# Performance work log

Hardware: AMD Instinct MI355X
Metric: run time of the kernel (lower is better)

Reference implementation:

```python
import jax, jax.numpy as jnp
from jax import lax
import numpy as np

VOCAB, TAGS, EMBED, HIDDEN, BATCH, SEQ = 50000, 9, 300, 1000, 32, 200


def setup_inputs() -> dict:
    key = jax.random.key(0)
    ks = jax.random.split(key, 12)
    s_e = 1.0 / np.sqrt(HIDDEN)
    inp = {
        "x": jax.random.randint(ks[0], (SEQ, BATCH), 0, VOCAB),
        "y": jax.random.randint(ks[1], (SEQ, BATCH), 0, TAGS),
        "embed_w": jax.random.normal(ks[2], (VOCAB, EMBED), jnp.float32),
        "W_ih": jax.random.uniform(ks[3], (4 * HIDDEN, EMBED), jnp.float32, -s_e, s_e),
        "W_hh": jax.random.uniform(ks[4], (4 * HIDDEN, HIDDEN), jnp.float32, -s_e, s_e),
        "b_ih": jax.random.uniform(ks[5], (4 * HIDDEN,), jnp.float32, -s_e, s_e),
        "b_hh": jax.random.uniform(ks[6], (4 * HIDDEN,), jnp.float32, -s_e, s_e),
        "lin_w": jax.random.uniform(ks[7], (TAGS, HIDDEN), jnp.float32, -s_e, s_e),
        "lin_b": jax.random.uniform(ks[8], (TAGS,), jnp.float32, -s_e, s_e),
        "start_trans": jax.random.uniform(ks[9], (TAGS,), jnp.float32, -0.1, 0.1),
        "end_trans": jax.random.uniform(ks[10], (TAGS,), jnp.float32, -0.1, 0.1),
        "trans": jax.random.uniform(ks[11], (TAGS, TAGS), jnp.float32, -0.1, 0.1),
    }
    return inp


def _forward(x, y, embed_w, W_ih, W_hh, b_ih, b_hh, lin_w, lin_b, start_trans, end_trans, trans):
    T, B = x.shape
    H = W_hh.shape[1]
    embeds = embed_w[x]  # [T,B,E]
    # Precompute input contribution to gates: [T,B,4H]
    xg = jnp.einsum("tbe,ge->tbg", embeds, W_ih) + b_ih + b_hh

    def lstm_step(carry, xg_t):
        h, c = carry
        g = xg_t + h @ W_hh.T  # [B,4H]
        i, f, gg, o = jnp.split(g, 4, axis=-1)  # PyTorch gate order i,f,g,o
        c = jax.nn.sigmoid(f) * c + jax.nn.sigmoid(i) * jnp.tanh(gg)
        h = jax.nn.sigmoid(o) * jnp.tanh(c)
        return (h, c), h

    h0 = jnp.zeros((B, H), embeds.dtype)
    _, hs = lax.scan(lstm_step, (h0, h0), xg)  # hs: [T,B,H]

    tag_space = jnp.einsum("tbh,kh->tbk", hs, lin_w) + lin_b  # [T,B,K]
    # Faithful to original: log_softmax over dim=1 (the batch axis)
    emissions = jax.nn.log_softmax(tag_space, axis=1)

    # ---- CRF log-likelihood (pytorch-crf semantics, full mask, sum reduction) ----
    b_idx = jnp.arange(B)
    em_at_y = jnp.take_along_axis(emissions, y[:, :, None], axis=2)[:, :, 0]  # [T,B]
    numerator = (
        start_trans[y[0]]
        + em_at_y.sum(axis=0)
        + trans[y[:-1], y[1:]].sum(axis=0)
        + end_trans[y[-1]]
    )  # [B]

    alpha0 = start_trans[None, :] + emissions[0]  # [B,K]

    def crf_step(alpha, em_t):
        # alpha: [B,K] over previous tag; em_t: [B,K]
        nxt = jax.nn.logsumexp(alpha[:, :, None] + trans[None, :, :] + em_t[:, None, :], axis=1)
        return nxt, None

    alpha, _ = lax.scan(crf_step, alpha0, emissions[1:])
    log_z = jax.nn.logsumexp(alpha + end_trans[None, :], axis=1)  # [B]
    return (numerator - log_z).sum()


def reference(x, y, embed_w, W_ih, W_hh, b_ih, b_hh, lin_w, lin_b, start_trans, end_trans, trans):
    return _forward(x, y, embed_w, W_ih, W_hh, b_ih, b_hh, lin_w, lin_b, start_trans, end_trans, trans)
```

## Files before the change

kernel.cpp:

```cpp
#include <hip/hip_runtime.h>

#define T_SEQ 200
#define NB    32
#define NE    300
#define NH    1000
#define NK    9
#define NJ    4096
#define EPD   320
#define WSCALE 256.0f
#define HSCALE 16.0f
#define LSCALE 512.0f
#define GSCALE (1.0f / (256.0f * 16.0f))
#define TSCALE (1.0f / (16.0f * 512.0f))

typedef __attribute__((ext_vector_type(4))) float f32x4;
typedef __attribute__((ext_vector_type(8))) short s16x8;
typedef __attribute__((ext_vector_type(4))) short s16x4;
typedef unsigned long long u64;

__device__ __forceinline__ unsigned short f2bf(float f) {
    union { float f; unsigned u; } v; v.f = f;
    unsigned r = v.u + 0x7FFFu + ((v.u >> 16) & 1u);
    return (unsigned short)(r >> 16);
}
__device__ __forceinline__ float bf2f(unsigned short h) {
    union { unsigned u; float f; } v; v.u = ((unsigned)h) << 16;
    return v.f;
}
__device__ __forceinline__ float ftanh(float x) {
    float e = __expf(fminf(2.f * x, 80.f));
    return (e - 1.f) / (e + 1.f);
}
__device__ __forceinline__ float fsig(float x) {
    return 1.f / (1.f + __expf(-x));
}
__device__ __forceinline__ unsigned nt_poll(const unsigned* p) {
    unsigned r;
    asm volatile("global_load_dword %0, %1, off nt\n\t"
                 "s_waitcnt vmcnt(0)"
                 : "=v"(r) : "v"(p) : "memory");
    return r;
}
__device__ __forceinline__ void plain_pub(unsigned* p, unsigned v) {
    __hip_atomic_store(p, v, __ATOMIC_RELAXED, __HIP_MEMORY_SCOPE_WORKGROUP);
}

__global__ __launch_bounds__(256) void prep_emb(
    const int* __restrict__ x, const float* __restrict__ embed_w,
    unsigned short* __restrict__ emb_bf, unsigned* __restrict__ ctrl)
{
    const int t = blockIdx.x, tid = threadIdx.x;
    if (blockIdx.x == 0) {
        for (int i = tid; i < 2048; i += 256)
            ctrl[i] = (i == 61) ? 0xffffffffu : 0u;
    }
    for (int idx = tid; idx < NB * EPD; idx += 256) {
        int b = idx / EPD, e = idx - b * EPD;
        float v = (e < NE) ? embed_w[(size_t)x[t * NB + b] * NE + e] : 0.f;
        emb_bf[((size_t)t * NB + b) * EPD + e] = f2bf(v);
    }
}

__global__ __launch_bounds__(256) void prep_w(
    const float* __restrict__ W_ih, const float* __restrict__ b_ih,
    const float* __restrict__ b_hh, const float* __restrict__ lin_w,
    unsigned short* __restrict__ wih_bf, float* __restrict__ biasg,
    unsigned char* __restrict__ linw_q)
{
    const int blk = blockIdx.x, tid = threadIdx.x;
    for (int idx = tid; idx < 64 * EPD; idx += 256) {
        int jr = idx / EPD, e = idx - jr * EPD;
        int jp = blk * 64 + jr;
        int wgu = jp >> 7, rr = jp & 127, g = rr >> 5, uu = rr & 31;
        int m = wgu * 32 + uu;
        float v = (m < NH && e < NE) ? W_ih[(size_t)(g * NH + m) * NE + e] : 0.f;
        wih_bf[(size_t)jp * EPD + e] = f2bf(v);
    }
    if (tid < 64) {
        int jp = blk * 64 + tid;
        int wgu = jp >> 7, rr = jp & 127, g = rr >> 5, uu = rr & 31;
        int m = wgu * 32 + uu;
        biasg[jp] = (m < NH) ? (b_ih[g * NH + m] + b_hh[g * NH + m]) : 0.f;
    }
    if (blk < 16) {
        int n = blk, k = tid * 4;
        float v0 = (n < NK && k + 0 < NH) ? lin_w[(size_t)n * NH + k + 0] * LSCALE : 0.f;
        float v1 = (n < NK && k + 1 < NH) ? lin_w[(size_t)n * NH + k + 1] * LSCALE : 0.f;
        float v2 = (n < NK && k + 2 < NH) ? lin_w[(size_t)n * NH + k + 2] * LSCALE : 0.f;
        float v3 = (n < NK && k + 3 < NH) ? lin_w[(size_t)n * NH + k + 3] * LSCALE : 0.f;
        int p01 = __builtin_amdgcn_cvt_pk_fp8_f32(v0, v1, 0, false);
        int p23 = __builtin_amdgcn_cvt_pk_fp8_f32(v2, v3, 0, false);
        ((unsigned*)linw_q)[n * 256 + tid] =
            ((unsigned)p01 & 0xffffu) | ((unsigned)p23 << 16);
    }
}

__device__ __forceinline__ int gate_xg(unsigned* done, int ready, int tn, int lane) {
    while (ready <= tn) {
        unsigned v = 64u;
        if (lane < 8 && ready + lane < T_SEQ)
            v = __hip_atomic_load(&done[ready + lane], __ATOMIC_RELAXED,
                                  __HIP_MEMORY_SCOPE_AGENT);
        unsigned m = (unsigned)__ballot((int)(v >= 64u)) & 255u;
        if (m & 1u) {
            unsigned run = (m == 255u) ? 8u : (unsigned)__builtin_ctz(~m);
            ready += (int)run;
        } else {
            __builtin_amdgcn_s_sleep(1);
        }
    }
    return ready;
}

__global__ __launch_bounds__(256, 1) void lstm_kernel(
    const float* __restrict__ W_hh,
    const unsigned short* __restrict__ emb_bf,
    const unsigned short* __restrict__ wih_bf,
    const float* __restrict__ biasg,
    unsigned short* __restrict__ xg,
    unsigned char* __restrict__ h_q,
    unsigned* __restrict__ ctrl)
{
    __shared__ __align__(16) unsigned char s_w[128 * 1024];
    __shared__ int s_chunk, s_grp, s_pid, s_mode;

    const int tid = threadIdx.x;

    if (tid == 0) {
        unsigned xcc;
        asm volatile("s_getreg_b32 %0, hwreg(HW_REG_XCC_ID)" : "=s"(xcc));
        xcc &= 15u;
        unsigned myidx = __hip_atomic_fetch_add(&ctrl[40 + xcc], 1u,
                             __ATOMIC_RELAXED, __HIP_MEMORY_SCOPE_AGENT);
        __threadfence();
        unsigned tot = __hip_atomic_fetch_add(&ctrl[60], 1u,
                             __ATOMIC_RELAXED, __HIP_MEMORY_SCOPE_AGENT);
        if (tot == 255u) {
            __threadfence();
            unsigned w0 = 0xffu, w1 = 0xffu;
            for (unsigned xx = 0; xx < 16; ++xx) {
                unsigned cx = __hip_atomic_load(&ctrl[40 + xx], __ATOMIC_RELAXED,
                                                __HIP_MEMORY_SCOPE_AGENT);
                if (cx >= 32u) {
                    if (w0 == 0xffu) w0 = xx;
                    else { w1 = xx; break; }
                }
            }
            __hip_atomic_store(&ctrl[61], w0 | (w1 << 8), __ATOMIC_RELAXED,
                               __HIP_MEMORY_SCOPE_AGENT);
        }
        unsigned win;
        do {
            win = __hip_atomic_load(&ctrl[61], __ATOMIC_RELAXED,
                                    __HIP_MEMORY_SCOPE_AGENT);
        } while (win == 0xffffffffu);
        unsigned w0 = win & 0xffu, w1 = (win >> 8) & 0xffu;
        int grp = -1;
        if (xcc == w0 && myidx < 32u) grp = 0;
        else if (xcc == w1 && myidx < 32u) grp = 1;
        s_grp = grp;
        s_chunk = (grp >= 0) ? (int)myidx : -1;
        s_pid = (grp >= 0) ? -1
                     : (int)__hip_atomic_fetch_add(&ctrl[62], 1u,
                           __ATOMIC_RELAXED, __HIP_MEMORY_SCOPE_AGENT);
    }
    __syncthreads();
    const int chunk = s_chunk;
    const int w = tid >> 6, lane = tid & 63;
    const int col = lane & 15, quad = lane >> 4;
    unsigned* done = ctrl + 256;

    if (chunk < 0) {
        const int pid = s_pid;
        for (int g = pid; g < T_SEQ * 64; g += 192) {
            const int t = g >> 6, jt = g & 63;
            const unsigned short* eb = emb_bf + (size_t)t * NB * EPD;
            const unsigned short* wb = wih_bf + (size_t)(jt * 64 + w * 16 + col) * EPD;
            const unsigned short* ea0 = eb + (size_t)col * EPD;
            const unsigned short* ea1 = eb + (size_t)(16 + col) * EPD;

            f32x4 acc0 = {0.f, 0.f, 0.f, 0.f};
            f32x4 acc1 = {0.f, 0.f, 0.f, 0.f};
#pragma unroll
            for (int kc = 0; kc < EPD / 32; ++kc) {
                int ko = kc * 32 + quad * 8;
                s16x8 a0 = *(const s16x8*)&ea0[ko];
                s16x8 a1 = *(const s16x8*)&ea1[ko];
                s16x8 bb = *(const s16x8*)&wb[ko];
                acc0 = __builtin_amdgcn_mfma_f32_16x16x32_bf16(a0, bb, acc0, 0, 0, 0);
                acc1 = __builtin_amdgcn_mfma_f32_16x16x32_bf16(a1, bb, acc1, 0, 0, 0);
            }
            const int jp = jt * 64 + w * 16 + col;
            const float bi = biasg[jp];
            size_t base = ((size_t)t * NJ + jp) * NB;
            union { s16x4 v; u64 q; } p0, p1;
#pragma unroll
            for (int r = 0; r < 4; ++r) {
                p0.v[r] = (short)f2bf(acc0[r] + bi);
                p1.v[r] = (short)f2bf(acc1[r] + bi);
            }
            __hip_atomic_store((u64*)&xg[base + quad * 4], p0.q,
                               __ATOMIC_RELAXED, __HIP_MEMORY_SCOPE_AGENT);
            __hip_atomic_store((u64*)&xg[base + 16 + quad * 4], p1.q,
                               __ATOMIC_RELAXED, __HIP_MEMORY_SCOPE_AGENT);
            __syncthreads();
            if (tid == 0)
                __hip_atomic_fetch_add(&done[t], 1u, __ATOMIC_RELAXED,
                                       __HIP_MEMORY_SCOPE_AGENT);
        }
        return;
    }

    const int grp = s_grp;
    const size_t GOFF = (size_t)grp * 16384;
    unsigned* fastf = ctrl + 64 + grp * 64;
    unsigned* slowf = ctrl + grp * 96;
    unsigned* s_w32 = (unsigned*)s_w;

    for (int idx = tid; idx < 128 * 256; idx += 256) {
        int r = idx >> 8, dw = idx & 255;
        int g = r >> 5, uu = r & 31, m = chunk * 32 + uu;
        float4 w4 = make_float4(0.f, 0.f, 0.f, 0.f);
        if (m < NH && dw < 250)
            w4 = *(const float4*)&W_hh[(size_t)(g * NH + m) * NH + dw * 4];
        int p0 = __builtin_amdgcn_cvt_pk_fp8_f32(w4.x * WSCALE, w4.y * WSCALE, 0, false);
        int p1 = __builtin_amdgcn_cvt_pk_fp8_f32(w4.z * WSCALE, w4.w * WSCALE, 0, false);
        unsigned v = ((unsigned)p0 & 0xffffu) | ((unsigned)p1 << 16);
        int kb = dw >> 1;
        int kbs = kb ^ (r & 15);
        s_w32[r * 256 + (kbs << 1) + (dw & 1)] = v;
    }
    if (tid < 128)
        *(unsigned*)(h_q + GOFF + (size_t)chunk * 512 + tid * 4) = 0u;
    __syncthreads();
    if (tid == 0) {
        plain_pub(&fastf[chunk], 1u);
        __hip_atomic_store(&slowf[chunk], 1u, __ATOMIC_RELAXED,
                           __HIP_MEMORY_SCOPE_AGENT);
    }
    if (grp == 0 && chunk == 0) {
        if (tid < 64) {
            int mode = 2;
            for (int it = 0; it < 8192; ++it) {
                unsigned v = (lane < 32) ? nt_poll(&fastf[lane]) : 1u;
                if (__all((int)(v >= 1u))) { mode = 1; break; }
            }
            if (tid == 0) {
                __hip_atomic_store(&ctrl[63], (unsigned)mode, __ATOMIC_RELAXED,
                                   __HIP_MEMORY_SCOPE_AGENT);
                s_mode = mode;
            }
        }
    } else {
        if (tid == 0) {
            unsigned m;
            do {
                m = __hip_atomic_load(&ctrl[63], __ATOMIC_RELAXED,
                                      __HIP_MEMORY_SCOPE_AGENT);
            } while (m == 0u);
            s_mode = (int)m;
        }
    }
    __syncthreads();
    const int mode = s_mode;

    if (w >= 2) {
        for (int t = 0; t < T_SEQ; ++t) __syncthreads();
        return;
    }
    const int p = w;

    int ready = 0;
    ready = gate_xg(done, ready, 0, lane);
    s16x4 xcur[4], xnxt[4];
#pragma unroll
    for (int g = 0; g < 4; ++g)
        xcur[g] = *(const s16x4*)&xg[((size_t)0 * NJ + chunk * 128 + (2 * g + p) * 16 + col) * NB
                                     + grp * 16 + quad * 4];

    float c[4] = {0.f, 0.f, 0.f, 0.f};
    const int rw = quad * 4;
    const int boff = col * 32 + quad * 8;

    for (int t = 0; t < T_SEQ; ++t) {
        const unsigned need = (unsigned)(t + 1);
        if (mode == 1) {
            for (;;) {
                unsigned v = (lane < 32) ? nt_poll(&fastf[lane]) : need;
                if (__all((int)(v >= need))) break;
            }
        } else {
            for (;;) {
                unsigned v = (lane < 32)
                    ? __hip_atomic_load(&slowf[lane], __ATOMIC_RELAXED,
                                        __HIP_MEMORY_SCOPE_AGENT)
                    : need;
                if (__all((int)(v >= need))) break;
            }
        }
        asm volatile("" ::: "memory");

        const unsigned char* pb = h_q + (size_t)t * 32768 + GOFF + boff;
        u64 a[32];
#pragma unroll
        for (int kc = 0; kc < 32; ++kc)
            a[kc] = *(const u64*)(pb + (size_t)kc * 512);

        if (t + 1 < T_SEQ) {
            ready = gate_xg(done, ready, t + 1, lane);
#pragma unroll
            for (int g = 0; g < 4; ++g)
                xnxt[g] = *(const s16x4*)&xg[((size_t)(t + 1) * NJ + chunk * 128 + (2 * g + p) * 16 + col) * NB
                                             + grp * 16 + quad * 4];
        }

        f32x4 acc0 = {0.f, 0.f, 0.f, 0.f};
        f32x4 acc1 = {0.f, 0.f, 0.f, 0.f};
        f32x4 acc2 = {0.f, 0.f, 0.f, 0.f};
        f32x4 acc3 = {0.f, 0.f, 0.f, 0.f};
#pragma unroll
        for (int kc = 0; kc < 32; ++kc) {
            int kb = kc * 4 + quad;
            u64 b0 = *(const u64*)&s_w[((0 * 2 + p) * 16 + col) * 1024 + ((kb ^ col) << 3)];
            u64 b1 = *(const u64*)&s_w[((1 * 2 + p) * 16 + col) * 1024 + ((kb ^ col) << 3)];
            u64 b2 = *(const u64*)&s_w[((2 * 2 + p) * 16 + col) * 1024 + ((kb ^ col) << 3)];
            u64 b3 = *(const u64*)&s_w[((3 * 2 + p) * 16 + col) * 1024 + ((kb ^ col) << 3)];
            acc0 = __builtin_amdgcn_mfma_f32_16x16x32_fp8_fp8((long)a[kc], (long)b0, acc0, 0, 0, 0);
            acc1 = __builtin_amdgcn_mfma_f32_16x16x32_fp8_fp8((long)a[kc], (long)b1, acc1, 0, 0, 0);
            acc2 = __builtin_amdgcn_mfma_f32_16x16x32_fp8_fp8((long)a[kc], (long)b2, acc2, 0, 0, 0);
            acc3 = __builtin_amdgcn_mfma_f32_16x16x32_fp8_fp8((long)a[kc], (long)b3, acc3, 0, 0, 0);
        }

        float hv[4];
#pragma unroll
        for (int r = 0; r < 4; ++r) {
            float gi = acc0[r] * GSCALE + bf2f((unsigned short)xcur[0][r]);
            float gf = acc1[r] * GSCALE + bf2f((unsigned short)xcur[1][r]);
            float gg = acc2[r] * GSCALE + bf2f((unsigned short)xcur[2][r]);
            float go = acc3[r] * GSCALE + bf2f((unsigned short)xcur[3][r]);
            c[r] = fsig(gf) * c[r] + fsig(gi) * ftanh(gg);
            hv[r] = fsig(go) * ftanh(c[r]);
        }
        {
            int p01 = __builtin_amdgcn_cvt_pk_fp8_f32(hv[0] * HSCALE, hv[1] * HSCALE, 0, false);
            int p23 = __builtin_amdgcn_cvt_pk_fp8_f32(hv[2] * HSCALE, hv[3] * HSCALE, 0, false);
            unsigned char* pg = h_q + (size_t)(t + 1) * 32768 + GOFF + (size_t)chunk * 512
                              + p * 16 + col;
            pg[(rw + 0) * 32] = (unsigned char)(p01 & 0xff);
            pg[(rw + 1) * 32] = (unsigned char)((p01 >> 8) & 0xff);
            pg[(rw + 2) * 32] = (unsigned char)(p23 & 0xff);
            pg[(rw + 3) * 32] = (unsigned char)((p23 >> 8) & 0xff);
        }
        __syncthreads();
        if (tid == 0) {
            plain_pub(&fastf[chunk], (unsigned)(t + 2));
            if (mode == 2)
                __hip_atomic_store(&slowf[chunk], (unsigned)(t + 2),
                                   __ATOMIC_RELAXED, __HIP_MEMORY_SCOPE_AGENT);
        }
#pragma unroll
        for (int g = 0; g < 4; ++g) xcur[g] = xnxt[g];
    }
}

__global__ __launch_bounds__(64) void tag_gemm(
    const unsigned char* __restrict__ h_q,
    const unsigned char* __restrict__ linw_q, float* __restrict__ ts)
{
    const int m0 = blockIdx.x * 16, lane = threadIdx.x;
    const int col = lane & 15, quad = lane >> 4;
    const int m = m0 + col, t = m >> 5, b = m & 31;
    const int g = b >> 4, bl = b & 15;
    const unsigned char* pa = h_q + (size_t)(t + 1) * 32768 + (size_t)g * 16384
                            + bl * 32 + quad * 8;
    const unsigned char* pw = linw_q + (size_t)col * 1024 + quad * 8;

    f32x4 acc = {0.f, 0.f, 0.f, 0.f};
#pragma unroll 8
    for (int kc = 0; kc < 32; ++kc) {
        u64 a  = *(const u64*)(pa + (size_t)kc * 512);
        u64 bv = *(const u64*)(pw + kc * 32);
        acc = __builtin_amdgcn_mfma_f32_16x16x32_fp8_fp8((long)a, (long)bv, acc, 0, 0, 0);
    }
#pragma unroll
    for (int r = 0; r < 4; ++r)
        ts[(size_t)(m0 + quad * 4 + r) * 16 + col] = acc[r] * TSCALE;
}

__global__ __launch_bounds__(320) void em_kernel(
    const float* __restrict__ ts, const float* __restrict__ lin_b,
    float* __restrict__ em)
{
    __shared__ float s_ts[NB * NK];
    __shared__ float s_lse[NK];
    const int t = blockIdx.x, tid = threadIdx.x;
    float val = 0.f;
    int b = tid / NK, k = tid - b * NK;
    if (tid < NB * NK) {
        val = ts[(size_t)(t * NB + b) * 16 + k] + lin_b[k];
        s_ts[b * NK + k] = val;
    }
    __syncthreads();
    if (tid < NK) {
        float m = -1e30f;
        for (int bb = 0; bb < NB; ++bb) m = fmaxf(m, s_ts[bb * NK + tid]);
        float s = 0.f;
        for (int bb = 0; bb < NB; ++bb) s += __expf(s_ts[bb * NK + tid] - m);
        s_lse[tid] = m + __logf(s);
    }
    __syncthreads();
    if (tid < NB * NK)
        em[((size_t)t * NB + b) * NK + k] = val - s_lse[k];
}

__global__ __launch_bounds__(320) void crf_kernel(
    const int* __restrict__ y, const float* __restrict__ em,
    const float* __restrict__ start_trans, const float* __restrict__ end_trans,
    const float* __restrict__ trans, float* __restrict__ out)
{
    __shared__ float s_trans[NK * NK];
    __shared__ float s_alpha[NB * NK];
    __shared__ float s_red[NB];
    const int tid = threadIdx.x;
    if (tid < NK * NK) s_trans[tid] = trans[tid];
    __syncthreads();

    float num = 0.f;
    if (tid < NB) {
        int b = tid, yp = y[b];
        num = start_trans[yp] + em[(size_t)b * NK + yp];
        for (int t = 1; t < T_SEQ; ++t) {
            int yc = y[t * NB + b];
            num += s_trans[yp * NK + yc] + em[((size_t)t * NB + b) * NK + yc];
            yp = yc;
        }
        num += end_trans[yp];
    }

    const int b = tid / NK, k = tid - (tid / NK) * NK;
    if (tid < NB * NK)
        s_alpha[tid] = start_trans[k] + em[(size_t)b * NK + k];
    __syncthreads();

    for (int t = 1; t < T_SEQ; ++t) {
        float nv = 0.f;
        if (tid < NB * NK) {
            float m = -1e30f;
#pragma unroll
            for (int i = 0; i < NK; ++i)
                m = fmaxf(m, s_alpha[b * NK + i] + s_trans[i * NK + k]);
            float s = 0.f;
#pragma unroll
            for (int i = 0; i < NK; ++i)
                s += __expf(s_alpha[b * NK + i] + s_trans[i * NK + k] - m);
            nv = em[((size_t)t * NB + b) * NK + k] + m + __logf(s);
        }
        __syncthreads();
        if (tid < NB * NK) s_alpha[tid] = nv;
        __syncthreads();
    }

    if (tid < NB) {
        float m = -1e30f;
        for (int k2 = 0; k2 < NK; ++k2)
            m = fmaxf(m, s_alpha[tid * NK + k2] + end_trans[k2]);
        float s = 0.f;
        for (int k2 = 0; k2 < NK; ++k2)
            s += __expf(s_alpha[tid * NK + k2] + end_trans[k2] - m);
        s_red[tid] = num - (m + __logf(s));
    }
    __syncthreads();
    if (tid == 0) {
        float tot = 0.f;
        for (int i = 0; i < NB; ++i) tot += s_red[i];
        out[0] = tot;
    }
}

extern "C" void kernel_launch(void* const* d_in, const int* in_sizes, int n_in,
                              void* d_out, int out_size, void* d_ws, size_t ws_size,
                              hipStream_t stream)
{
    const int*   x           = (const int*)d_in[0];
    const int*   y           = (const int*)d_in[1];
    const float* embed_w     = (const float*)d_in[2];
    const float* W_ih        = (const float*)d_in[3];
    const float* W_hh        = (const float*)d_in[4];
    const float* b_ih        = (const float*)d_in[5];
    const float* b_hh        = (const float*)d_in[6];
    const float* lin_w       = (const float*)d_in[7];
    const float* lin_b       = (const float*)d_in[8];
    const float* start_trans = (const float*)d_in[9];
    const float* end_trans   = (const float*)d_in[10];
    const float* trans       = (const float*)d_in[11];
    float* out = (float*)d_out;

    char* ws = (char*)d_ws;
    unsigned short* xg     = (unsigned short*)(ws);
    float*          ts     = (float*)(ws);
    unsigned char*  h_q    = (unsigned char*)(ws + 52428800);
    unsigned char*  linw_q = (unsigned char*)(ws + 59015168);
    float*          em     = (float*)(ws + 65601536);
    unsigned*       ctrl   = (unsigned*)(ws + 65831936);
    float*          biasg  = (float*)(ws + 65840128);
    unsigned short* emb_bf = (unsigned short*)(ws + 65856512);
    unsigned short* wih_bf = (unsigned short*)(ws + 69952512);

    prep_emb<<<dim3(T_SEQ), 256, 0, stream>>>(x, embed_w, emb_bf, ctrl);
    prep_w<<<dim3(64), 256, 0, stream>>>(W_ih, b_ih, b_hh, lin_w, wih_bf, biasg, linw_q);

    lstm_kernel<<<dim3(256), 256, 0, stream>>>(W_hh, emb_bf, wih_bf, biasg,
                                               xg, h_q, ctrl);

    tag_gemm<<<dim3(400), 64, 0, stream>>>(h_q, linw_q, ts);
    em_kernel<<<dim3(T_SEQ), 320, 0, stream>>>(ts, lin_b, em);
    crf_kernel<<<dim3(1), 320, 0, stream>>>(y, em, start_trans, end_trans, trans, out);
}
```

Before: 1.040 ms.

## Replace per-chunk flag polling with L2 atomic counter and offload xg prefetch to idle waves

Cross-block step synchronization now uses a single per-group counter incremented with an L2 atomic add and polled by one wave with sleeps, instead of 32 lanes polling per-chunk flags. The previously idle waves 2-3 prefetch the next step's input-gate values into a double-buffered LDS tile, so the compute waves no longer do global xg loads. This adds an extra __syncthreads per step and always writes the slow flag as a fallback. The intent is less poll traffic and a shorter critical path per recurrent step.

```diff
diff --git a/kernel.cpp b/kernel.cpp
--- a/kernel.cpp
+++ b/kernel.cpp
@@ -34,15 +34,16 @@
 __device__ __forceinline__ float fsig(float x) {
     return 1.f / (1.f + __expf(-x));
 }
-__device__ __forceinline__ unsigned nt_poll(const unsigned* p) {
+__device__ __forceinline__ void l2_add1(unsigned* p) {
+    asm volatile("global_atomic_add %0, %1, off"
+                 :: "v"(p), "v"(1u) : "memory");
+}
+__device__ __forceinline__ unsigned l2_poll(const unsigned* p) {
     unsigned r;
-    asm volatile("global_load_dword %0, %1, off nt\n\t"
+    asm volatile("global_load_dword %0, %1, off sc0 nt\n\t"
                  "s_waitcnt vmcnt(0)"
                  : "=v"(r) : "v"(p) : "memory");
     return r;
-}
-__device__ __forceinline__ void plain_pub(unsigned* p, unsigned v) {
-    __hip_atomic_store(p, v, __ATOMIC_RELAXED, __HIP_MEMORY_SCOPE_WORKGROUP);
 }
 
 __global__ __launch_bounds__(256) void prep_emb(
@@ -122,6 +123,7 @@
     unsigned* __restrict__ ctrl)
 {
     __shared__ __align__(16) unsigned char s_w[128 * 1024];
+    __shared__ __align__(16) unsigned char s_xg[2][4096];
     __shared__ int s_chunk, s_grp, s_pid, s_mode;
 
     const int tid = threadIdx.x;
@@ -213,8 +215,8 @@
 
     const int grp = s_grp;
     const size_t GOFF = (size_t)grp * 16384;
-    unsigned* fastf = ctrl + 64 + grp * 64;
     unsigned* slowf = ctrl + grp * 96;
+    unsigned* cnt   = ctrl + 64 + grp * 96;
     unsigned* s_w32 = (unsigned*)s_w;
 
     for (int idx = tid; idx < 128 * 256; idx += 256) {
@@ -234,21 +236,21 @@
         *(unsigned*)(h_q + GOFF + (size_t)chunk * 512 + tid * 4) = 0u;
     __syncthreads();
     if (tid == 0) {
-        plain_pub(&fastf[chunk], 1u);
+        l2_add1(cnt);
         __hip_atomic_store(&slowf[chunk], 1u, __ATOMIC_RELAXED,
                            __HIP_MEMORY_SCOPE_AGENT);
     }
     if (grp == 0 && chunk == 0) {
-        if (tid < 64) {
-            int mode = 2;
-            for (int it = 0; it < 8192; ++it) {
-                unsigned v = (lane < 32) ? nt_poll(&fastf[lane]) : 1u;
-                if (__all((int)(v >= 1u))) { mode = 1; break; }
+        if (w == 0) {
+            int md = 2;
+            for (int it = 0; it < 4096; ++it) {
+                if (l2_poll(cnt) >= 32u) { md = 1; break; }
+                __builtin_amdgcn_s_sleep(1);
             }
             if (tid == 0) {
-                __hip_atomic_store(&ctrl[63], (unsigned)mode, __ATOMIC_RELAXED,
+                __hip_atomic_store(&ctrl[63], (unsigned)md, __ATOMIC_RELAXED,
                                    __HIP_MEMORY_SCOPE_AGENT);
-                s_mode = mode;
+                s_mode = md;
             }
         }
     } else {
@@ -264,102 +266,120 @@
     __syncthreads();
     const int mode = s_mode;
 
-    if (w >= 2) {
-        for (int t = 0; t < T_SEQ; ++t) __syncthreads();
-        return;
-    }
-    const int p = w;
-
-    int ready = 0;
-    ready = gate_xg(done, ready, 0, lane);
-    s16x4 xcur[4], xnxt[4];
-#pragma unroll
-    for (int g = 0; g < 4; ++g)
-        xcur[g] = *(const s16x4*)&xg[((size_t)0 * NJ + chunk * 128 + (2 * g + p) * 16 + col) * NB
-                                     + grp * 16 + quad * 4];
-
+    const int p = w & 1;
     float c[4] = {0.f, 0.f, 0.f, 0.f};
     const int rw = quad * 4;
     const int boff = col * 32 + quad * 8;
+    int ready23 = 0;
+
+    if (w >= 2) {
+        ready23 = gate_xg(done, 0, 0, lane);
+        const int idx128 = tid - 128;
+        const size_t rb = ((size_t)0 * NJ + chunk * 128 + idx128) * NB + grp * 16;
+        unsigned char* db = &s_xg[0][idx128 * 32];
+#pragma unroll
+        for (int bq = 0; bq < 4; ++bq)
+            *(u64*)(db + bq * 8) = *(const u64*)&xg[rb + bq * 4];
+    }
 
     for (int t = 0; t < T_SEQ; ++t) {
-        const unsigned need = (unsigned)(t + 1);
-        if (mode == 1) {
-            for (;;) {
-                unsigned v = (lane < 32) ? nt_poll(&fastf[lane]) : need;
-                if (__all((int)(v >= need))) break;
+        if (w == 0) {
+            const unsigned need = (unsigned)(t + 1);
+            if (mode == 1) {
+                const unsigned need32 = 32u * need;
+                int it = 0;
+                for (;;) {
+                    if (l2_poll(cnt) >= need32) break;
+                    if (++it >= 65536) {
+                        unsigned v = (lane < 32)
+                            ? __hip_atomic_load(&slowf[lane], __ATOMIC_RELAXED,
+                                                __HIP_MEMORY_SCOPE_AGENT)
+                            : need;
+                        if (__all((int)(v >= need))) break;
+                        it = 0;
+                    }
+                    __builtin_amdgcn_s_sleep(1);
+                }
+            } else {
+                for (;;) {
+                    unsigned v = (lane < 32)
+                        ? __hip_atomic_load(&slowf[lane], __ATOMIC_RELAXED,
+                                            __HIP_MEMORY_SCOPE_AGENT)
+                        : need;
+                    if (__all((int)(v >= need))) break;
+                }
+            }
+            asm volatile("" ::: "memory");
+        }
+        __syncthreads();
+
+        if (w < 2) {
+            const unsigned char* pb = h_q + (size_t)t * 32768 + GOFF + boff;
+            u64 a[32];
+#pragma unroll
+            for (int kc = 0; kc < 32; ++kc)
+                a[kc] = *(const u64*)(pb + (size_t)kc * 512);
+
+            f32x4 acc0 = {0.f, 0.f, 0.f, 0.f};
+            f32x4 acc1 = {0.f, 0.f, 0.f, 0.f};
+            f32x4 acc2 = {0.f, 0.f, 0.f, 0.f};
+            f32x4 acc3 = {0.f, 0.f, 0.f, 0.f};
+#pragma unroll
+            for (int kc = 0; kc < 32; ++kc) {
+                int kb = kc * 4 + quad;
+                u64 b0 = *(const u64*)&s_w[((0 * 2 + p) * 16 + col) * 1024 + ((kb ^ col) << 3)];
+                u64 b1 = *(const u64*)&s_w[((1 * 2 + p) * 16 + col) * 1024 + ((kb ^ col) << 3)];
+                u64 b2 = *(const u64*)&s_w[((2 * 2 + p) * 16 + col) * 1024 + ((kb ^ col) << 3)];
+                u64 b3 = *(const u64*)&s_w[((3 * 2 + p) * 16 + col) * 1024 + ((kb ^ col) << 3)];
+                acc0 = __builtin_amdgcn_mfma_f32_16x16x32_fp8_fp8((long)a[kc], (long)b0, acc0, 0, 0, 0);
+                acc1 = __builtin_amdgcn_mfma_f32_16x16x32_fp8_fp8((long)a[kc], (long)b1, acc1, 0, 0, 0);
+                acc2 = __builtin_amdgcn_mfma_f32_16x16x32_fp8_fp8((long)a[kc], (long)b2, acc2, 0, 0, 0);
+                acc3 = __builtin_amdgcn_mfma_f32_16x16x32_fp8_fp8((long)a[kc], (long)b3, acc3, 0, 0, 0);
+            }
+
+            const unsigned char* xb = &s_xg[t & 1][0];
+            s16x4 xc[4];
+#pragma unroll
+            for (int g = 0; g < 4; ++g)
+                xc[g] = *(const s16x4*)&xb[(((2 * g + p) * 16 + col) * 32) + quad * 8];
+
+            float hv[4];
+#pragma unroll
+            for (int r = 0; r < 4; ++r) {
+                float gi = acc0[r] * GSCALE + bf2f((unsigned short)xc[0][r]);
+                float gf = acc1[r] * GSCALE + bf2f((unsigned short)xc[1][r]);
+                float gg = acc2[r] * GSCALE + bf2f((unsigned short)xc[2][r]);
+                float go = acc3[r] * GSCALE + bf2f((unsigned short)xc[3][r]);
+                c[r] = fsig(gf) * c[r] + fsig(gi) * ftanh(gg);
+                hv[r] = fsig(go) * ftanh(c[r]);
+            }
+            {
+                int p01 = __builtin_amdgcn_cvt_pk_fp8_f32(hv[0] * HSCALE, hv[1] * HSCALE, 0, false);
+                int p23 = __builtin_amdgcn_cvt_pk_fp8_f32(hv[2] * HSCALE, hv[3] * HSCALE, 0, false);
+                unsigned char* pg = h_q + (size_t)(t + 1) * 32768 + GOFF + (size_t)chunk * 512
+                                  + p * 16 + col;
+                pg[(rw + 0) * 32] = (unsigned char)(p01 & 0xff);
+                pg[(rw + 1) * 32] = (unsigned char)((p01 >> 8) & 0xff);
+                pg[(rw + 2) * 32] = (unsigned char)(p23 & 0xff);
+                pg[(rw + 3) * 32] = (unsigned char)((p23 >> 8) & 0xff);
             }
         } else {
-            for (;;) {
-                unsigned v = (lane < 32)
-                    ? __hip_atomic_load(&slowf[lane], __ATOMIC_RELAXED,
-                                        __HIP_MEMORY_SCOPE_AGENT)
-                    : need;
-                if (__all((int)(v >= need))) break;
-            }
-        }
-        asm volatile("" ::: "memory");
-
-        const unsigned char* pb = h_q + (size_t)t * 32768 + GOFF + boff;
-        u64 a[32];
-#pragma unroll
-        for (int kc = 0; kc < 32; ++kc)
-            a[kc] = *(const u64*)(pb + (size_t)kc * 512);
-
-        if (t + 1 < T_SEQ) {
-            ready = gate_xg(done, ready, t + 1, lane);
-#pragma unroll
-            for (int g = 0; g < 4; ++g)
-                xnxt[g] = *(const s16x4*)&xg[((size_t)(t + 1) * NJ + chunk * 128 + (2 * g + p) * 16 + col) * NB
-                                             + grp * 16 + quad * 4];
-        }
-
-        f32x4 acc0 = {0.f, 0.f, 0.f, 0.f};
-        f32x4 acc1 = {0.f, 0.f, 0.f, 0.f};
-        f32x4 acc2 = {0.f, 0.f, 0.f, 0.f};
-        f32x4 acc3 = {0.f, 0.f, 0.f, 0.f};
-#pragma unroll
-        for (int kc = 0; kc < 32; ++kc) {
-            int kb = kc * 4 + quad;
-            u64 b0 = *(const u64*)&s_w[((0 * 2 + p) * 16 + col) * 1024 + ((kb ^ col) << 3)];
-            u64 b1 = *(const u64*)&s_w[((1 * 2 + p) * 16 + col) * 1024 + ((kb ^ col) << 3)];
-            u64 b2 = *(const u64*)&s_w[((2 * 2 + p) * 16 + col) * 1024 + ((kb ^ col) << 3)];
-            u64 b3 = *(const u64*)&s_w[((3 * 2 + p) * 16 + col) * 1024 + ((kb ^ col) << 3)];
-            acc0 = __builtin_amdgcn_mfma_f32_16x16x32_fp8_fp8((long)a[kc], (long)b0, acc0, 0, 0, 0);
-            acc1 = __builtin_amdgcn_mfma_f32_16x16x32_fp8_fp8((long)a[kc], (long)b1, acc1, 0, 0, 0);
-            acc2 = __builtin_amdgcn_mfma_f32_16x16x32_fp8_fp8((long)a[kc], (long)b2, acc2, 0, 0, 0);
-            acc3 = __builtin_amdgcn_mfma_f32_16x16x32_fp8_fp8((long)a[kc], (long)b3, acc3, 0, 0, 0);
-        }
-
-        float hv[4];
-#pragma unroll
-        for (int r = 0; r < 4; ++r) {
-            float gi = acc0[r] * GSCALE + bf2f((unsigned short)xcur[0][r]);
-            float gf = acc1[r] * GSCALE + bf2f((unsigned short)xcur[1][r]);
-            float gg = acc2[r] * GSCALE + bf2f((unsigned short)xcur[2][r]);
-            float go = acc3[r] * GSCALE + bf2f((unsigned short)xcur[3][r]);
-            c[r] = fsig(gf) * c[r] + fsig(gi) * ftanh(gg);
-            hv[r] = fsig(go) * ftanh(c[r]);
-        }
-        {
-            int p01 = __builtin_amdgcn_cvt_pk_fp8_f32(hv[0] * HSCALE, hv[1] * HSCALE, 0, false);
-            int p23 = __builtin_amdgcn_cvt_pk_fp8_f32(hv[2] * HSCALE, hv[3] * HSCALE, 0, false);
-            unsigned char* pg = h_q + (size_t)(t + 1) * 32768 + GOFF + (size_t)chunk * 512
-                              + p * 16 + col;
-            pg[(rw + 0) * 32] = (unsigned char)(p01 & 0xff);
-            pg[(rw + 1) * 32] = (unsigned char)((p01 >> 8) & 0xff);
-            pg[(rw + 2) * 32] = (unsigned char)(p23 & 0xff);
-            pg[(rw + 3) * 32] = (unsigned char)((p23 >> 8) & 0xff);
+            if (t + 1 < T_SEQ) {
+                ready23 = gate_xg(done, ready23, t + 1, lane);
+                const int idx128 = tid - 128;
+                const size_t rb = ((size_t)(t + 1) * NJ + chunk * 128 + idx128) * NB + grp * 16;
+                unsigned char* db = &s_xg[(t + 1) & 1][idx128 * 32];
+#pragma unroll
+                for (int bq = 0; bq < 4; ++bq)
+                    *(u64*)(db + bq * 8) = *(const u64*)&xg[rb + bq * 4];
+            }
         }
         __syncthreads();
         if (tid == 0) {
-            plain_pub(&fastf[chunk], (unsigned)(t + 2));
-            if (mode == 2)
-                __hip_atomic_store(&slowf[chunk], (unsigned)(t + 2),
-                                   __ATOMIC_RELAXED, __HIP_MEMORY_SCOPE_AGENT);
-        }
-#pragma unroll
-        for (int g = 0; g < 4; ++g) xcur[g] = xnxt[g];
+            l2_add1(cnt);
+            __hip_atomic_store(&slowf[chunk], (unsigned)(t + 2),
+                               __ATOMIC_RELAXED, __HIP_MEMORY_SCOPE_AGENT);
+        }
     }
 }
 
```

Result: slower. 1.194 ms (+14.8%).

## Replace per-step block barrier with per-wave flags and fold xg gating into poll

Applied to the files above, without the earlier changes.

Each of the two active waves in a recurrent block now publishes its own progress flag after a vmcnt wait, instead of the whole block hitting __syncthreads and one thread publishing. The two idle waves simply exit rather than looping through barriers. The xg readiness check is merged into the h-polling spin loop with a two-step lookahead, so it no longer runs as a separate gate. Control words are relocated to avoid overlap with the wider flag arrays. The intent is to shorten the per-timestep critical path of the serial LSTM. The cost is more flags to poll, and correctness now rests on per-wave memory ordering.

```diff
diff --git a/kernel.cpp b/kernel.cpp
--- a/kernel.cpp
+++ b/kernel.cpp
@@ -52,7 +52,7 @@
     const int t = blockIdx.x, tid = threadIdx.x;
     if (blockIdx.x == 0) {
         for (int i = tid; i < 2048; i += 256)
-            ctrl[i] = (i == 61) ? 0xffffffffu : 0u;
+            ctrl[i] = (i == 497) ? 0xffffffffu : 0u;
     }
     for (int idx = tid; idx < NB * EPD; idx += 256) {
         int b = idx / EPD, e = idx - b * EPD;
@@ -130,28 +130,28 @@
         unsigned xcc;
         asm volatile("s_getreg_b32 %0, hwreg(HW_REG_XCC_ID)" : "=s"(xcc));
         xcc &= 15u;
-        unsigned myidx = __hip_atomic_fetch_add(&ctrl[40 + xcc], 1u,
+        unsigned myidx = __hip_atomic_fetch_add(&ctrl[480 + xcc], 1u,
                              __ATOMIC_RELAXED, __HIP_MEMORY_SCOPE_AGENT);
         __threadfence();
-        unsigned tot = __hip_atomic_fetch_add(&ctrl[60], 1u,
+        unsigned tot = __hip_atomic_fetch_add(&ctrl[496], 1u,
                              __ATOMIC_RELAXED, __HIP_MEMORY_SCOPE_AGENT);
         if (tot == 255u) {
             __threadfence();
             unsigned w0 = 0xffu, w1 = 0xffu;
             for (unsigned xx = 0; xx < 16; ++xx) {
-                unsigned cx = __hip_atomic_load(&ctrl[40 + xx], __ATOMIC_RELAXED,
+                unsigned cx = __hip_atomic_load(&ctrl[480 + xx], __ATOMIC_RELAXED,
                                                 __HIP_MEMORY_SCOPE_AGENT);
                 if (cx >= 32u) {
                     if (w0 == 0xffu) w0 = xx;
                     else { w1 = xx; break; }
                 }
             }
-            __hip_atomic_store(&ctrl[61], w0 | (w1 << 8), __ATOMIC_RELAXED,
+            __hip_atomic_store(&ctrl[497], w0 | (w1 << 8), __ATOMIC_RELAXED,
                                __HIP_MEMORY_SCOPE_AGENT);
         }
         unsigned win;
         do {
-            win = __hip_atomic_load(&ctrl[61], __ATOMIC_RELAXED,
+            win = __hip_atomic_load(&ctrl[497], __ATOMIC_RELAXED,
                                     __HIP_MEMORY_SCOPE_AGENT);
         } while (win == 0xffffffffu);
         unsigned w0 = win & 0xffu, w1 = (win >> 8) & 0xffu;
@@ -161,7 +161,7 @@
         s_grp = grp;
         s_chunk = (grp >= 0) ? (int)myidx : -1;
         s_pid = (grp >= 0) ? -1
-                     : (int)__hip_atomic_fetch_add(&ctrl[62], 1u,
+                     : (int)__hip_atomic_fetch_add(&ctrl[498], 1u,
                            __ATOMIC_RELAXED, __HIP_MEMORY_SCOPE_AGENT);
     }
     __syncthreads();
@@ -213,8 +213,8 @@
 
     const int grp = s_grp;
     const size_t GOFF = (size_t)grp * 16384;
-    unsigned* fastf = ctrl + 64 + grp * 64;
-    unsigned* slowf = ctrl + grp * 96;
+    unsigned* slowf = ctrl + grp * 64;
+    unsigned* fastf = ctrl + 128 + grp * 64;
     unsigned* s_w32 = (unsigned*)s_w;
 
     for (int idx = tid; idx < 128 * 256; idx += 256) {
@@ -234,44 +234,40 @@
         *(unsigned*)(h_q + GOFF + (size_t)chunk * 512 + tid * 4) = 0u;
     __syncthreads();
     if (tid == 0) {
-        plain_pub(&fastf[chunk], 1u);
-        __hip_atomic_store(&slowf[chunk], 1u, __ATOMIC_RELAXED,
+        plain_pub(&fastf[chunk * 2 + 0], 1u);
+        plain_pub(&fastf[chunk * 2 + 1], 1u);
+        __hip_atomic_store(&slowf[chunk * 2 + 0], 1u, __ATOMIC_RELAXED,
                            __HIP_MEMORY_SCOPE_AGENT);
-    }
-    if (grp == 0 && chunk == 0) {
-        if (tid < 64) {
-            int mode = 2;
-            for (int it = 0; it < 8192; ++it) {
-                unsigned v = (lane < 32) ? nt_poll(&fastf[lane]) : 1u;
-                if (__all((int)(v >= 1u))) { mode = 1; break; }
-            }
-            if (tid == 0) {
-                __hip_atomic_store(&ctrl[63], (unsigned)mode, __ATOMIC_RELAXED,
-                                   __HIP_MEMORY_SCOPE_AGENT);
-                s_mode = mode;
-            }
-        }
-    } else {
-        if (tid == 0) {
-            unsigned m;
-            do {
-                m = __hip_atomic_load(&ctrl[63], __ATOMIC_RELAXED,
-                                      __HIP_MEMORY_SCOPE_AGENT);
-            } while (m == 0u);
-            s_mode = (int)m;
-        }
+        __hip_atomic_store(&slowf[chunk * 2 + 1], 1u, __ATOMIC_RELAXED,
+                           __HIP_MEMORY_SCOPE_AGENT);
+    }
+    if (grp == 0 && chunk == 0 && w == 0) {
+        int md = 2;
+        for (int it = 0; it < 8192; ++it) {
+            unsigned v = nt_poll(&fastf[lane]);
+            if (__all((int)(v >= 1u))) { md = 1; break; }
+        }
+        if (lane == 0) {
+            __hip_atomic_store(&ctrl[499], (unsigned)md, __ATOMIC_RELAXED,
+                               __HIP_MEMORY_SCOPE_AGENT);
+            s_mode = md;
+        }
+    } else if (tid == 0) {
+        unsigned m;
+        do {
+            m = __hip_atomic_load(&ctrl[499], __ATOMIC_RELAXED,
+                                  __HIP_MEMORY_SCOPE_AGENT);
+        } while (m == 0u);
+        s_mode = (int)m;
     }
     __syncthreads();
     const int mode = s_mode;
 
-    if (w >= 2) {
-        for (int t = 0; t < T_SEQ; ++t) __syncthreads();
-        return;
-    }
+    if (w >= 2) return;
     const int p = w;
-
-    int ready = 0;
-    ready = gate_xg(done, ready, 0, lane);
+    const int fid = chunk * 2 + w;
+
+    int ready = gate_xg(done, 0, 1, lane);
     s16x4 xcur[4], xnxt[4];
 #pragma unroll
     for (int g = 0; g < 4; ++g)
@@ -284,18 +280,40 @@
 
     for (int t = 0; t < T_SEQ; ++t) {
         const unsigned need = (unsigned)(t + 1);
+        const int gt = t + 2;
+        bool gate_pending = (gt < T_SEQ) && (ready <= gt);
         if (mode == 1) {
             for (;;) {
-                unsigned v = (lane < 32) ? nt_poll(&fastf[lane]) : need;
-                if (__all((int)(v >= need))) break;
+                unsigned v = nt_poll(&fastf[lane]);
+                bool hok = __all((int)(v >= need));
+                if (gate_pending) {
+                    unsigned d = 64u;
+                    if (lane < 8 && ready + lane < T_SEQ)
+                        d = __hip_atomic_load(&done[ready + lane], __ATOMIC_RELAXED,
+                                              __HIP_MEMORY_SCOPE_AGENT);
+                    unsigned m = (unsigned)__ballot((int)(d >= 64u)) & 255u;
+                    if (m & 1u)
+                        ready += (m == 255u) ? 8 : (int)__builtin_ctz(~m);
+                    gate_pending = (ready <= gt);
+                }
+                if (hok && !gate_pending) break;
             }
         } else {
             for (;;) {
-                unsigned v = (lane < 32)
-                    ? __hip_atomic_load(&slowf[lane], __ATOMIC_RELAXED,
-                                        __HIP_MEMORY_SCOPE_AGENT)
-                    : need;
-                if (__all((int)(v >= need))) break;
+                unsigned v = __hip_atomic_load(&slowf[lane], __ATOMIC_RELAXED,
+                                               __HIP_MEMORY_SCOPE_AGENT);
+                bool hok = __all((int)(v >= need));
+                if (gate_pending) {
+                    unsigned d = 64u;
+                    if (lane < 8 && ready + lane < T_SEQ)
+                        d = __hip_atomic_load(&done[ready + lane], __ATOMIC_RELAXED,
+                                              __HIP_MEMORY_SCOPE_AGENT);
+                    unsigned m = (unsigned)__ballot((int)(d >= 64u)) & 255u;
+                    if (m & 1u)
+                        ready += (m == 255u) ? 8 : (int)__builtin_ctz(~m);
+                    gate_pending = (ready <= gt);
+                }
+                if (hok && !gate_pending) break;
             }
         }
         asm volatile("" ::: "memory");
@@ -307,7 +325,6 @@
             a[kc] = *(const u64*)(pb + (size_t)kc * 512);
 
         if (t + 1 < T_SEQ) {
-            ready = gate_xg(done, ready, t + 1, lane);
 #pragma unroll
             for (int g = 0; g < 4; ++g)
                 xnxt[g] = *(const s16x4*)&xg[((size_t)(t + 1) * NJ + chunk * 128 + (2 * g + p) * 16 + col) * NB
@@ -351,11 +368,11 @@
             pg[(rw + 2) * 32] = (unsigned char)(p23 & 0xff);
             pg[(rw + 3) * 32] = (unsigned char)((p23 >> 8) & 0xff);
         }
-        __syncthreads();
-        if (tid == 0) {
-            plain_pub(&fastf[chunk], (unsigned)(t + 2));
+        asm volatile("s_waitcnt vmcnt(0)" ::: "memory");
+        if (lane == 0) {
+            plain_pub(&fastf[fid], (unsigned)(t + 2));
             if (mode == 2)
-                __hip_atomic_store(&slowf[chunk], (unsigned)(t + 2),
+                __hip_atomic_store(&slowf[fid], (unsigned)(t + 2),
                                    __ATOMIC_RELAXED, __HIP_MEMORY_SCOPE_AGENT);
         }
 #pragma unroll
```

After: 1.054 ms. No clear change (+1.4%).
